# Kernel tuning notes

Measured on AMD Instinct MI355X. Metric: run time of the kernel, lower is better.

The kernel has to match this reference:

```python
import jax, jax.numpy as jnp
import numpy as np

B, T = 32, 64
DETER, HID, STOCH, CLASSES = 2048, 1024, 32, 32
ACT, EMB, BLOCKS = 16, 1024, 8
FLAT = STOCH * CLASSES
DPB = DETER // BLOCKS
DYN_IN_PB = DPB + 3 * HID
EPS = 1e-6
UNIMIX = 0.01


def _rms(x, g):
    return x * jax.lax.rsqrt(jnp.mean(x * x, axis=-1, keepdims=True) + EPS) * g


def _block_linear(x, W, b):
    # x: [N, BLOCKS*in_pb], W: [BLOCKS, in_pb, out_pb] -> [N, BLOCKS*out_pb]
    xg = x.reshape(x.shape[0], BLOCKS, -1)
    y = jnp.einsum('nbi,bio->nbo', xg, W)
    return y.reshape(x.shape[0], -1) + b


def setup_inputs() -> dict:
    key = jax.random.key(0)
    ks = iter(jax.random.split(key, 64))
    def lin(i, o):
        return jax.random.normal(next(ks), (i, o), jnp.float32) / np.float32(np.sqrt(i))
    inp = {}
    inp['embed'] = jax.random.normal(next(ks), (B, T, EMB), jnp.float32)
    inp['action'] = jax.random.normal(next(ks), (B, T, ACT), jnp.float32)
    inp['is_first'] = jax.random.randint(next(ks), (B, T), 0, 2).astype(jnp.int32)
    inp['W_in_deter'] = lin(DETER, HID); inp['b_in_deter'] = jnp.zeros((HID,), jnp.float32); inp['g_in_deter'] = jnp.ones((HID,), jnp.float32)
    inp['W_in_stoch'] = lin(FLAT, HID); inp['b_in_stoch'] = jnp.zeros((HID,), jnp.float32); inp['g_in_stoch'] = jnp.ones((HID,), jnp.float32)
    inp['W_in_act'] = lin(ACT, HID); inp['b_in_act'] = jnp.zeros((HID,), jnp.float32); inp['g_in_act'] = jnp.ones((HID,), jnp.float32)
    inp['W_dyn'] = jax.random.normal(next(ks), (BLOCKS, DYN_IN_PB, DPB), jnp.float32) / np.float32(np.sqrt(DYN_IN_PB))
    inp['b_dyn'] = jnp.zeros((DETER,), jnp.float32); inp['g_dyn'] = jnp.ones((DETER,), jnp.float32)
    inp['W_gru'] = jax.random.normal(next(ks), (BLOCKS, DPB, 3 * DPB), jnp.float32) / np.float32(np.sqrt(DPB))
    inp['b_gru'] = jnp.zeros((3 * DETER,), jnp.float32)
    inp['W_p0'] = lin(DETER, HID); inp['b_p0'] = jnp.zeros((HID,), jnp.float32); inp['g_p0'] = jnp.ones((HID,), jnp.float32)
    inp['W_p1'] = lin(HID, HID); inp['b_p1'] = jnp.zeros((HID,), jnp.float32); inp['g_p1'] = jnp.ones((HID,), jnp.float32)
    inp['W_po'] = jax.random.uniform(next(ks), (HID, FLAT), jnp.float32, -1.0, 1.0) / np.float32(np.sqrt(HID))
    inp['b_po'] = jnp.zeros((FLAT,), jnp.float32)
    inp['W_q0'] = lin(DETER + EMB, HID); inp['b_q0'] = jnp.zeros((HID,), jnp.float32); inp['g_q0'] = jnp.ones((HID,), jnp.float32)
    inp['W_qo'] = jax.random.uniform(next(ks), (HID, FLAT), jnp.float32, -1.0, 1.0) / np.float32(np.sqrt(HID))
    inp['b_qo'] = jnp.zeros((FLAT,), jnp.float32)
    return inp


def reference(embed, action, is_first,
              W_in_deter, b_in_deter, g_in_deter,
              W_in_stoch, b_in_stoch, g_in_stoch,
              W_in_act, b_in_act, g_in_act,
              W_dyn, b_dyn, g_dyn, W_gru, b_gru,
              W_p0, b_p0, g_p0, W_p1, b_p1, g_p1, W_po, b_po,
              W_q0, b_q0, g_q0, W_qo, b_qo):

    def core(deter, stoch_flat, act):
        denom = jax.lax.stop_gradient(jnp.maximum(jnp.abs(act), 1.0))
        a = act / denom
        x0 = jax.nn.silu(_rms(deter @ W_in_deter + b_in_deter, g_in_deter))
        x1 = jax.nn.silu(_rms(stoch_flat @ W_in_stoch + b_in_stoch, g_in_stoch))
        x2 = jax.nn.silu(_rms(a @ W_in_act + b_in_act, g_in_act))
        x = jnp.concatenate([x0, x1, x2], axis=-1)  # [B, 3H]
        xb = jnp.broadcast_to(x[:, None, :], (x.shape[0], BLOCKS, 3 * HID))
        dg = deter.reshape(-1, BLOCKS, DPB)
        h = jnp.concatenate([dg, xb], axis=-1).reshape(x.shape[0], -1)
        h = jax.nn.silu(_rms(_block_linear(h, W_dyn, b_dyn), g_dyn))
        gates = _block_linear(h, W_gru, b_gru).reshape(-1, BLOCKS, 3 * DPB)
        r = jax.nn.sigmoid(gates[..., :DPB])
        c = jnp.tanh(r * gates[..., DPB:2 * DPB])
        u = jax.nn.sigmoid(gates[..., 2 * DPB:] - 1.0)
        return (u * c + (1.0 - u) * dg).reshape(-1, DETER)

    def prior(deter):
        x = jax.nn.silu(_rms(deter @ W_p0 + b_p0, g_p0))
        x = jax.nn.silu(_rms(x @ W_p1 + b_p1, g_p1))
        return (x @ W_po + b_po).reshape(-1, STOCH, CLASSES)

    def post(deter, emb):
        x = jnp.concatenate([deter, emb], axis=-1)
        x = jax.nn.silu(_rms(x @ W_q0 + b_q0, g_q0))
        return (x @ W_qo + b_qo).reshape(-1, STOCH, CLASSES)

    def mode_st(logits):
        # unimix categorical, deterministic mode with straight-through gradients
        probs = (1.0 - UNIMIX) * jax.nn.softmax(logits, axis=-1) + UNIMIX / CLASSES
        onehot = jax.nn.one_hot(jnp.argmax(probs, axis=-1), CLASSES, dtype=probs.dtype)
        return onehot + probs - jax.lax.stop_gradient(probs)

    def step(carry, xs):
        deter, stoch = carry
        emb_t, act_t, first_t = xs
        m = (1.0 - first_t.astype(jnp.float32))[:, None]
        deter = deter * m
        stoch = stoch * m
        act_t = act_t * m
        deter = core(deter, stoch, act_t)
        prior_logits = prior(deter)
        post_logits = post(deter, emb_t)
        stoch = mode_st(post_logits).reshape(-1, FLAT)
        return (deter, stoch), (post_logits, prior_logits, deter)

    carry0 = (jnp.zeros((B, DETER), embed.dtype), jnp.zeros((B, FLAT), embed.dtype))
    xs = (embed.transpose(1, 0, 2), action.transpose(1, 0, 2), is_first.T)
    _, (post_l, prior_l, deters) = jax.lax.scan(step, carry0, xs)
    return (post_l.transpose(1, 0, 2, 3), prior_l.transpose(1, 0, 2, 3), deters.transpose(1, 0, 2))
```

## Files before the change

kernel.cpp:

```cpp
#include <hip/hip_runtime.h>
#include <math.h>

#define DEVINL __device__ __forceinline__
typedef float f32x4 __attribute__((ext_vector_type(4)));


struct RPtrs {
  const float *embed, *action; const int *is_first;
  const float *W_in_deter, *b_in_deter, *g_in_deter;
  const float *W_in_stoch, *b_in_stoch, *g_in_stoch;
  const float *W_in_act,   *b_in_act,   *g_in_act;
  const float *W_dyn, *b_dyn, *g_dyn;
  const float *W_gru, *b_gru;
  const float *W_p0, *b_p0, *g_p0;
  const float *W_p1, *b_p1, *g_p1;
  const float *W_po, *b_po;
  const float *W_q0, *b_q0, *g_q0;
  const float *W_qo, *b_qo;
  float *out_post, *out_prior, *out_deters;
  float *deter, *determ, *xact, *hact;
  float *SDyn, *SQ0, *SX0, *Abuf0, *Abuf1;
  int *sidxg;
};

struct LdPlain {
  const float* A; int lda;
  DEVINL const float* addr(int r, int k) const { return A + (size_t)r * lda + k; }
};
struct LdDyn {
  const float* dm; const float* x; int blk;
  DEVINL const float* addr(int r, int k) const {
    return (k < 256) ? dm + (size_t)r * 2048 + blk * 256 + k
                     : x + (size_t)r * 3072 + (k - 256);
  }
};
struct LdQ0 {
  const float* det; const float* emb; int t;
  DEVINL const float* addr(int r, int k) const {
    return (k < 2048) ? det + (size_t)r * 2048 + k
                      : emb + ((size_t)r * 64 + t) * 1024 + (k - 2048);
  }
};

#define FMA4(A, S, W) { (A)[0]=fmaf((S),(W)[0],(A)[0]); (A)[1]=fmaf((S),(W)[1],(A)[1]); \
                        (A)[2]=fmaf((S),(W)[2],(A)[2]); (A)[3]=fmaf((S),(W)[3],(A)[3]); }

template <int NBLK, typename LA>
DEVINL void gemm_tile(LA la, const float* __restrict__ W, int ldw, int wcb,
                      int k0, float* __restrict__ slab, int sst, int scb,
                      const float* __restrict__ bias, float* As) {
  const int tid = threadIdx.x;
  const int c4 = (tid & 63) * 4;
  const int rg = (tid >> 6) * 8;
  const int srr = tid & 31;
  const int skk = (tid >> 5) * 8;
  f32x4 acc[8];
#pragma unroll
  for (int i = 0; i < 8; ++i) acc[i] = (f32x4){0.f, 0.f, 0.f, 0.f};
  const float* ap = la.addr(srr, k0 + skk);
  f32x4 cur0 = *(const f32x4*)ap;
  f32x4 cur1 = *(const f32x4*)(ap + 4);
#pragma unroll
  for (int b = 0; b < NBLK; ++b) {
    __syncthreads();
#pragma unroll
    for (int e = 0; e < 4; ++e) {
      As[(skk + e) * 36 + srr]     = cur0[e];
      As[(skk + 4 + e) * 36 + srr] = cur1[e];
    }
    f32x4 nxt0, nxt1;
    if (b + 1 < NBLK) {
      const float* np = la.addr(srr, k0 + (b + 1) * 64 + skk);
      nxt0 = *(const f32x4*)np;
      nxt1 = *(const f32x4*)(np + 4);
    }
    __syncthreads();
    const float* Wp = W + (size_t)(k0 + b * 64) * ldw + wcb + c4;
#pragma unroll 8
    for (int kk = 0; kk < 64; ++kk) {
      f32x4 w = *(const f32x4*)(Wp + (size_t)kk * ldw);
      const float* Ab = As + kk * 36 + rg;
      f32x4 alo = *(const f32x4*)(Ab);
      f32x4 ahi = *(const f32x4*)(Ab + 4);
      FMA4(acc[0], alo[0], w); FMA4(acc[1], alo[1], w);
      FMA4(acc[2], alo[2], w); FMA4(acc[3], alo[3], w);
      FMA4(acc[4], ahi[0], w); FMA4(acc[5], ahi[1], w);
      FMA4(acc[6], ahi[2], w); FMA4(acc[7], ahi[3], w);
    }
    if (b + 1 < NBLK) { cur0 = nxt0; cur1 = nxt1; }
  }
  f32x4 bv = (f32x4){0.f, 0.f, 0.f, 0.f};
  if (bias) bv = *(const f32x4*)(bias + wcb + c4);
#pragma unroll
  for (int i = 0; i < 8; ++i) {
    f32x4 o = acc[i] + bv;
    *(f32x4*)(slab + (size_t)(rg + i) * sst + scb + c4) = o;
  }
}

template <typename LA>
DEVINL void gemm_big(LA la, const float* __restrict__ W, int ldw, int wcb,
                     int nblk, float* __restrict__ outp, int ost,
                     const float* __restrict__ bias, float* As) {
  const int tid = threadIdx.x;
  const int c4 = (tid & 63) * 4;
  const int rg = (tid >> 6) * 8;
  const int srr = tid & 31;
  const int skk = (tid >> 5) * 8;
  f32x4 acc[8];
#pragma unroll
  for (int i = 0; i < 8; ++i) acc[i] = (f32x4){0.f, 0.f, 0.f, 0.f};
  const float* ap = la.addr(srr, skk);
  f32x4 cur0 = *(const f32x4*)ap;
  f32x4 cur1 = *(const f32x4*)(ap + 4);
  f32x4 nxt0, nxt1;
  for (int b = 0; b < nblk; ++b) {
    __syncthreads();
#pragma unroll
    for (int e = 0; e < 4; ++e) {
      As[(skk + e) * 36 + srr]     = cur0[e];
      As[(skk + 4 + e) * 36 + srr] = cur1[e];
    }
    if (b + 1 < nblk) {
      const float* np = la.addr(srr, (b + 1) * 64 + skk);
      nxt0 = *(const f32x4*)np;
      nxt1 = *(const f32x4*)(np + 4);
    }
    __syncthreads();
    const float* Wp = W + (size_t)(b * 64) * ldw + wcb + c4;
#pragma unroll 8
    for (int kk = 0; kk < 64; ++kk) {
      f32x4 w = *(const f32x4*)(Wp + (size_t)kk * ldw);
      const float* Ab = As + kk * 36 + rg;
      f32x4 alo = *(const f32x4*)(Ab);
      f32x4 ahi = *(const f32x4*)(Ab + 4);
      FMA4(acc[0], alo[0], w); FMA4(acc[1], alo[1], w);
      FMA4(acc[2], alo[2], w); FMA4(acc[3], alo[3], w);
      FMA4(acc[4], ahi[0], w); FMA4(acc[5], ahi[1], w);
      FMA4(acc[6], ahi[2], w); FMA4(acc[7], ahi[3], w);
    }
    if (b + 1 < nblk) { cur0 = nxt0; cur1 = nxt1; }
  }
  f32x4 bv = *(const f32x4*)(bias + wcb + c4);
#pragma unroll
  for (int i = 0; i < 8; ++i) {
    f32x4 o = acc[i] + bv;
    *(f32x4*)(outp + (size_t)(rg + i) * ost + wcb + c4) = o;
  }
}

DEVINL void act_fin(const float* __restrict__ slab, int N, int nch, int r,
                    const float* __restrict__ g, float* __restrict__ out,
                    float invN, float* red) {
  const int tid = threadIdx.x;
  const size_t cstr = (size_t)32 * N;
  const float* base = slab + (size_t)r * N + tid * 4;
  f32x4 y0 = (f32x4){0.f, 0.f, 0.f, 0.f}, y1 = y0;
  for (int ch = 0; ch < nch; ++ch)
    y0 += *(const f32x4*)(base + (size_t)ch * cstr);
  float ss = y0[0]*y0[0] + y0[1]*y0[1] + y0[2]*y0[2] + y0[3]*y0[3];
  if (N == 2048) {
    for (int ch = 0; ch < nch; ++ch)
      y1 += *(const f32x4*)(base + 1024 + (size_t)ch * cstr);
    ss += y1[0]*y1[0] + y1[1]*y1[1] + y1[2]*y1[2] + y1[3]*y1[3];
  }
#pragma unroll
  for (int o = 32; o > 0; o >>= 1) ss += __shfl_down(ss, o, 64);
  if ((tid & 63) == 0) red[tid >> 6] = ss;
  __syncthreads();
  if (tid == 0)
    red[4] = 1.f / sqrtf((red[0] + red[1] + red[2] + red[3]) * invN + 1e-6f);
  __syncthreads();
  const float sc = red[4];
  {
    f32x4 gg = *(const f32x4*)(g + tid * 4);
    f32x4 v = y0 * sc * gg;
#pragma unroll
    for (int k = 0; k < 4; ++k) v[k] = v[k] / (1.f + expf(-v[k]));
    *(f32x4*)(out + tid * 4) = v;
  }
  if (N == 2048) {
    f32x4 gg = *(const f32x4*)(g + 1024 + tid * 4);
    f32x4 v = y1 * sc * gg;
#pragma unroll
    for (int k = 0; k < 4; ++k) v[k] = v[k] / (1.f + expf(-v[k]));
    *(f32x4*)(out + 1024 + tid * 4) = v;
  }
}

DEVINL float sigm(float x) { return 1.f / (1.f + expf(-x)); }

DEVINL void x2_row(const RPtrs& p, int tt, int r, float m, float* red) {
  const int tid = threadIdx.x;
  const int c0 = tid * 4;
  const float* arow = p.action + ((size_t)r * 64 + tt) * 16;
  f32x4 s2 = *(const f32x4*)(p.b_in_act + c0);
#pragma unroll
  for (int ii = 0; ii < 16; ++ii) {
    float av = arow[ii] * m;
    av = av / fmaxf(fabsf(av), 1.f);
    f32x4 wv = *(const f32x4*)(p.W_in_act + ii * 1024 + c0);
    FMA4(s2, av, wv);
  }
  float ss = s2[0]*s2[0] + s2[1]*s2[1] + s2[2]*s2[2] + s2[3]*s2[3];
#pragma unroll
  for (int o = 32; o > 0; o >>= 1) ss += __shfl_down(ss, o, 64);
  if ((tid & 63) == 0) red[tid >> 6] = ss;
  __syncthreads();
  if (tid == 0)
    red[4] = 1.f / sqrtf((red[0] + red[1] + red[2] + red[3]) * (1.f / 1024.f) + 1e-6f);
  __syncthreads();
  float sc = red[4];
  f32x4 gg = *(const f32x4*)(p.g_in_act + c0);
  f32x4 v = s2 * sc * gg;
#pragma unroll
  for (int k = 0; k < 4; ++k) v[k] = v[k] / (1.f + expf(-v[k]));
  *(f32x4*)(p.xact + (size_t)r * 3072 + 2048 + c0) = v;
}

DEVINL void bias_row(const float* __restrict__ b, const float* __restrict__ g,
                     float* __restrict__ out, float* red) {
  const int tid = threadIdx.x;
  const int c0 = tid * 4;
  f32x4 pre = *(const f32x4*)(b + c0);
  float ss = pre[0]*pre[0] + pre[1]*pre[1] + pre[2]*pre[2] + pre[3]*pre[3];
#pragma unroll
  for (int o = 32; o > 0; o >>= 1) ss += __shfl_down(ss, o, 64);
  if ((tid & 63) == 0) red[tid >> 6] = ss;
  __syncthreads();
  if (tid == 0)
    red[4] = 1.f / sqrtf((red[0] + red[1] + red[2] + red[3]) * (1.f / 1024.f) + 1e-6f);
  __syncthreads();
  float sc = red[4];
  f32x4 gg = *(const f32x4*)(g + c0);
  f32x4 v = pre * sc * gg;
#pragma unroll
  for (int k = 0; k < 4; ++k) v[k] = v[k] / (1.f + expf(-v[k]));
  *(f32x4*)(out + c0) = v;
}

__global__ __launch_bounds__(256) void k_init(RPtrs p) {
  __shared__ float red[8];
  const int wg = blockIdx.x;
  size_t i = (size_t)wg * 256 + threadIdx.x;
  if (i < 65536) { p.deter[i] = 0.f; p.determ[i] = 0.f; }
  if (wg >= 480) {
    const int r = wg - 480;
    bias_row(p.b_in_deter, p.g_in_deter, p.xact + (size_t)r * 3072, red);
    __syncthreads();
    bias_row(p.b_in_stoch, p.g_in_stoch, p.xact + (size_t)r * 3072 + 1024, red);
    __syncthreads();
    float m = p.is_first[r * 64] ? 0.f : 1.f;
    x2_row(p, 0, r, m, red);
  }
}

__global__ __launch_bounds__(256, 2) void k_dyn(RPtrs p, int t) {
  __shared__ __align__(16) float As[2304];
  const int wg = blockIdx.x;
  int blk = wg / 26, kc = wg % 26;
  LdDyn la{p.determ, p.xact, blk};
  gemm_tile<2>(la, p.W_dyn + (size_t)blk * 851968, 256, 0, kc * 128,
               p.SDyn + (size_t)kc * 65536, 2048, blk * 256,
               kc == 0 ? p.b_dyn + blk * 256 : nullptr, As);
}

__global__ __launch_bounds__(256, 2) void k_dynfin(RPtrs p) {
  __shared__ float red[8];
  act_fin(p.SDyn, 2048, 26, blockIdx.x, p.g_dyn,
          p.hact + (size_t)blockIdx.x * 2048, 1.f / 2048.f, red);
}

__global__ __launch_bounds__(256, 2) void k_gru(RPtrs p, int t) {
  __shared__ float Al[8704];
  const int wg = blockIdx.x;
  const int blk = wg >> 4, jch = wg & 15;
  const int tid = threadIdx.x;
  {
    const float* hp = p.hact + blk * 256 + tid;
#pragma unroll
    for (int jb = 0; jb < 32; ++jb)
      Al[tid * 34 + jb] = hp[(size_t)jb * 2048];
  }
  __syncthreads();
  const int j = tid & 15, rg = tid >> 4;
  const int r0 = rg * 2;
  const int jcol = jch * 16 + j;
  const float* Wg = p.W_gru + (size_t)blk * 196608 + jcol;
  float r0a = 0, r1a = 0, c0a = 0, c1a = 0, u0a = 0, u1a = 0;
#pragma unroll 4
  for (int kk = 0; kk < 256; ++kk) {
    float wr = Wg[(size_t)kk * 768];
    float wc = Wg[(size_t)kk * 768 + 256];
    float wu = Wg[(size_t)kk * 768 + 512];
    float ax = Al[kk * 34 + r0], ay = Al[kk * 34 + r0 + 1];
    r0a = fmaf(ax, wr, r0a); r1a = fmaf(ay, wr, r1a);
    c0a = fmaf(ax, wc, c0a); c1a = fmaf(ay, wc, c1a);
    u0a = fmaf(ax, wu, u0a); u1a = fmaf(ay, wu, u1a);
  }
  const int col = blk * 256 + jcol;
  const float br = p.b_gru[blk * 768 + jcol];
  const float bc = p.b_gru[blk * 768 + 256 + jcol];
  const float bu = p.b_gru[blk * 768 + 512 + jcol];
#pragma unroll
  for (int rr = 0; rr < 2; ++rr) {
    int r = r0 + rr;
    float gr = (rr ? r1a : r0a) + br;
    float gc = (rr ? c1a : c0a) + bc;
    float gu = (rr ? u1a : u0a) + bu;
    float rs = sigm(gr);
    float cc = tanhf(rs * gc);
    float uu = sigm(gu - 1.f);
    float dg = p.determ[(size_t)r * 2048 + col];
    float nd = uu * cc + (1.f - uu) * dg;
    p.deter[(size_t)r * 2048 + col] = nd;
    p.out_deters[((size_t)r * 64 + t) * 2048 + col] = nd;
    float mn = 0.f;
    if (t + 1 < 64) mn = p.is_first[r * 64 + (t + 1)] ? 0.f : 1.f;
    p.determ[(size_t)r * 2048 + col] = nd * mn;
  }
}

__global__ __launch_bounds__(256, 2) void k_q0x0(RPtrs p, int t) {
  __shared__ __align__(16) float As[2304];
  const int wg = blockIdx.x;
  if (wg < 96) {
    int ct = wg & 3, kc = wg >> 2;
    LdQ0 la{p.deter, p.embed, t};
    gemm_tile<2>(la, p.W_q0, 1024, ct * 256, kc * 128,
                 p.SQ0 + (size_t)kc * 32768, 1024, ct * 256,
                 kc == 0 ? p.b_q0 : nullptr, As);
  } else {
    if (t >= 63) return;
    int i = wg - 96, ct = i & 3, kc = i >> 2;
    LdPlain la{p.determ, 2048};
    gemm_tile<2>(la, p.W_in_deter, 1024, ct * 256, kc * 128,
                 p.SX0 + (size_t)kc * 32768, 1024, ct * 256,
                 kc == 0 ? p.b_in_deter : nullptr, As);
  }
}

__global__ __launch_bounds__(256, 2) void k_qo256(RPtrs p, int t) {
  __shared__ __align__(16) float smem[2184];
  float* qrow = smem;
  float* pbuf = smem + 1024;
  float* ybuf = smem + 2048;
  float* red  = smem + 2176;
  const int wg = blockIdx.x;
  const int r = wg >> 3, ch = wg & 7;
  const int tid = threadIdx.x;
  const int c0 = tid * 4;
  {
    const float* base = p.SQ0 + (size_t)r * 1024 + c0;
    f32x4 y = (f32x4){0.f, 0.f, 0.f, 0.f};
#pragma unroll
    for (int cc = 0; cc < 24; ++cc) y += *(const f32x4*)(base + (size_t)cc * 32768);
    float ss = y[0]*y[0] + y[1]*y[1] + y[2]*y[2] + y[3]*y[3];
#pragma unroll
    for (int o = 32; o > 0; o >>= 1) ss += __shfl_down(ss, o, 64);
    if ((tid & 63) == 0) red[tid >> 6] = ss;
    __syncthreads();
    if (tid == 0)
      red[4] = 1.f / sqrtf((red[0] + red[1] + red[2] + red[3]) * (1.f / 1024.f) + 1e-6f);
    __syncthreads();
    float sc = red[4];
    f32x4 gg = *(const f32x4*)(p.g_q0 + c0);
    f32x4 v = y * sc * gg;
#pragma unroll
    for (int k = 0; k < 4; ++k) v[k] = v[k] / (1.f + expf(-v[k]));
    *(f32x4*)(qrow + c0) = v;
  }
  __syncthreads();
  const int cg = tid & 31, ks = tid >> 5;
  {
    f32x4 acc = (f32x4){0.f, 0.f, 0.f, 0.f};
    const float* Wq = p.W_qo + ch * 128 + cg * 4;
    const float* qr = qrow + ks * 128;
#pragma unroll 8
    for (int k = 0; k < 128; ++k) {
      f32x4 wv = *(const f32x4*)(Wq + (size_t)(ks * 128 + k) * 1024);
      FMA4(acc, qr[k], wv);
    }
    *(f32x4*)(pbuf + (ks * 32 + cg) * 4) = acc;
  }
  __syncthreads();
  if (tid < 32) {
    f32x4 s = *(const f32x4*)(p.b_qo + ch * 128 + tid * 4);
#pragma unroll
    for (int k2 = 0; k2 < 8; ++k2) s += *(const f32x4*)(pbuf + (k2 * 32 + tid) * 4);
    *(f32x4*)(p.out_post + ((size_t)r * 64 + t) * 1024 + ch * 128 + tid * 4) = s;
    *(f32x4*)(ybuf + tid * 4) = s;
  }
  __syncthreads();
  if (t < 63 && tid < 4) {
    const float* rb = ybuf + tid * 32;
    float best = rb[0]; int bi = 0;
#pragma unroll
    for (int c = 1; c < 32; ++c) {
      float v = rb[c];
      if (v > best) { best = v; bi = c; }
    }
    p.sidxg[r * 32 + ch * 4 + tid] = bi;
  }
}

__global__ __launch_bounds__(256, 2) void k_finx12(RPtrs p, int t) {
  __shared__ float red[8];
  __shared__ int sidx[32];
  const int wg = blockIdx.x;
  const int tid = threadIdx.x;
  if (wg >= 32) {
    act_fin(p.SX0, 1024, 16, wg - 32, p.g_in_deter,
            p.xact + (size_t)(wg - 32) * 3072, 1.f / 1024.f, red);
    return;
  }
  const int r = wg;
  if (tid < 32) sidx[tid] = p.sidxg[r * 32 + tid] & 31;
  __syncthreads();
  const float m = p.is_first[r * 64 + t + 1] ? 0.f : 1.f;
  const int c0 = tid * 4;
  f32x4 s1 = (f32x4){0.f, 0.f, 0.f, 0.f};
  if (m != 0.f) {
    for (int g = 0; g < 32; ++g)
      s1 += *(const f32x4*)(p.W_in_stoch + (size_t)(g * 32 + sidx[g]) * 1024 + c0);
  }
  f32x4 pre = *(const f32x4*)(p.b_in_stoch + c0) + s1 * m;
  float ss = pre[0]*pre[0] + pre[1]*pre[1] + pre[2]*pre[2] + pre[3]*pre[3];
#pragma unroll
  for (int o = 32; o > 0; o >>= 1) ss += __shfl_down(ss, o, 64);
  if ((tid & 63) == 0) red[tid >> 6] = ss;
  __syncthreads();
  if (tid == 0)
    red[4] = 1.f / sqrtf((red[0] + red[1] + red[2] + red[3]) * (1.f / 1024.f) + 1e-6f);
  __syncthreads();
  {
    float sc = red[4];
    f32x4 gg = *(const f32x4*)(p.g_in_stoch + c0);
    f32x4 v = pre * sc * gg;
#pragma unroll
    for (int k = 0; k < 4; ++k) v[k] = v[k] / (1.f + expf(-v[k]));
    *(f32x4*)(p.xact + (size_t)r * 3072 + 1024 + c0) = v;
  }
  __syncthreads();
  x2_row(p, t + 1, r, m, red);
}

__global__ __launch_bounds__(256, 2) void kb_p0(RPtrs p) {
  __shared__ __align__(16) float As[2304];
  int rb = blockIdx.x >> 2, ct = blockIdx.x & 3;
  LdPlain la{p.out_deters + (size_t)rb * 32 * 2048, 2048};
  gemm_big(la, p.W_p0, 1024, ct * 256, 32,
           p.Abuf0 + (size_t)rb * 32 * 1024, 1024, p.b_p0, As);
}
__global__ __launch_bounds__(256, 2) void kb_fin0(RPtrs p) {
  __shared__ float red[8];
  int r = blockIdx.x;
  act_fin(p.Abuf0, 1024, 1, r, p.g_p0, p.Abuf1 + (size_t)r * 1024,
          1.f / 1024.f, red);
}
__global__ __launch_bounds__(256, 2) void kb_p1(RPtrs p) {
  __shared__ __align__(16) float As[2304];
  int rb = blockIdx.x >> 2, ct = blockIdx.x & 3;
  LdPlain la{p.Abuf1 + (size_t)rb * 32 * 1024, 1024};
  gemm_big(la, p.W_p1, 1024, ct * 256, 16,
           p.Abuf0 + (size_t)rb * 32 * 1024, 1024, p.b_p1, As);
}
__global__ __launch_bounds__(256, 2) void kb_fin1(RPtrs p) {
  __shared__ float red[8];
  int r = blockIdx.x;
  act_fin(p.Abuf0, 1024, 1, r, p.g_p1, p.Abuf1 + (size_t)r * 1024,
          1.f / 1024.f, red);
}
__global__ __launch_bounds__(256, 2) void kb_po(RPtrs p) {
  __shared__ __align__(16) float As[2304];
  int rb = blockIdx.x >> 2, ct = blockIdx.x & 3;
  LdPlain la{p.Abuf1 + (size_t)rb * 32 * 1024, 1024};
  gemm_big(la, p.W_po, 1024, ct * 256, 16,
           p.out_prior + (size_t)rb * 32 * 1024, 1024, p.b_po, As);
}

extern "C" void kernel_launch(void* const* d_in, const int* in_sizes, int n_in,
                              void* d_out, int out_size, void* d_ws,
                              size_t ws_size, hipStream_t stream) {
  RPtrs p;
  p.embed      = (const float*)d_in[0];
  p.action     = (const float*)d_in[1];
  p.is_first   = (const int*)d_in[2];
  p.W_in_deter = (const float*)d_in[3];  p.b_in_deter = (const float*)d_in[4];  p.g_in_deter = (const float*)d_in[5];
  p.W_in_stoch = (const float*)d_in[6];  p.b_in_stoch = (const float*)d_in[7];  p.g_in_stoch = (const float*)d_in[8];
  p.W_in_act   = (const float*)d_in[9];  p.b_in_act   = (const float*)d_in[10]; p.g_in_act   = (const float*)d_in[11];
  p.W_dyn      = (const float*)d_in[12]; p.b_dyn      = (const float*)d_in[13]; p.g_dyn      = (const float*)d_in[14];
  p.W_gru      = (const float*)d_in[15]; p.b_gru      = (const float*)d_in[16];
  p.W_p0       = (const float*)d_in[17]; p.b_p0       = (const float*)d_in[18]; p.g_p0       = (const float*)d_in[19];
  p.W_p1       = (const float*)d_in[20]; p.b_p1       = (const float*)d_in[21]; p.g_p1       = (const float*)d_in[22];
  p.W_po       = (const float*)d_in[23]; p.b_po       = (const float*)d_in[24];
  p.W_q0       = (const float*)d_in[25]; p.b_q0       = (const float*)d_in[26]; p.g_q0       = (const float*)d_in[27];
  p.W_qo       = (const float*)d_in[28]; p.b_qo       = (const float*)d_in[29];

  float* o = (float*)d_out;
  p.out_post   = o;
  p.out_prior  = o + 2097152;
  p.out_deters = o + 4194304;

  float* w = (float*)d_ws;
  p.deter  = w;
  p.determ = w + 65536;
  p.xact   = w + 131072;
  p.hact   = w + 229376;
  p.SDyn   = w + 393216;
  p.SQ0    = w + 2097152;
  p.SX0    = w + 2883584;
  p.Abuf0  = w;
  p.Abuf1  = w + 2097152;
  p.sidxg  = (int*)(w + 4194304);

  k_init<<<512, 256, 0, stream>>>(p);
  for (int t = 0; t < 64; ++t) {
    k_dyn<<<208, 256, 0, stream>>>(p, t);
    k_dynfin<<<32, 256, 0, stream>>>(p);
    k_gru<<<128, 256, 0, stream>>>(p, t);
    k_q0x0<<<160, 256, 0, stream>>>(p, t);
    k_qo256<<<256, 256, 0, stream>>>(p, t);
    if (t < 63) k_finx12<<<64, 256, 0, stream>>>(p, t);
  }
  kb_p0<<<256, 256, 0, stream>>>(p);
  kb_fin0<<<2048, 256, 0, stream>>>(p);
  kb_p1<<<256, 256, 0, stream>>>(p);
  kb_fin1<<<2048, 256, 0, stream>>>(p);
  kb_po<<<256, 256, 0, stream>>>(p);
}
```

Before: 6.935 ms.

## Enlarge post-scan GEMM row tile to 64 and move x0 finalize into qo kernel

The post-scan prior MLP GEMMs now compute 64 rows per block with 16 accumulators per thread instead of 32 rows, halving block count and doubling reuse of each weight load. The fin kernels each process 8 rows per block to cut block count. The in_deter act_fin work moves from k_finx12 into extra blocks of k_qo256, so it overlaps with the qo work and k_finx12 runs fewer blocks. The larger tile raises register pressure and lowers parallelism (128 blocks on a large GPU).

After: 7.397 ms. +6.7%, slower.

```diff
diff --git a/kernel.cpp b/kernel.cpp
--- a/kernel.cpp
+++ b/kernel.cpp
@@ -99,51 +99,63 @@
 }
 
 template <typename LA>
-DEVINL void gemm_big(LA la, const float* __restrict__ W, int ldw, int wcb,
-                     int nblk, float* __restrict__ outp, int ost,
-                     const float* __restrict__ bias, float* As) {
+DEVINL void gemm_big64(LA la, const float* __restrict__ W, int ldw, int wcb,
+                       int nblk, float* __restrict__ outp, int ost,
+                       const float* __restrict__ bias, float* As) {
   const int tid = threadIdx.x;
   const int c4 = (tid & 63) * 4;
-  const int rg = (tid >> 6) * 8;
-  const int srr = tid & 31;
-  const int skk = (tid >> 5) * 8;
-  f32x4 acc[8];
-#pragma unroll
-  for (int i = 0; i < 8; ++i) acc[i] = (f32x4){0.f, 0.f, 0.f, 0.f};
+  const int rg = (tid >> 6) * 16;
+  const int srr = tid & 63;
+  const int skk = (tid >> 6) * 16;
+  f32x4 acc[16];
+#pragma unroll
+  for (int i = 0; i < 16; ++i) acc[i] = (f32x4){0.f, 0.f, 0.f, 0.f};
   const float* ap = la.addr(srr, skk);
   f32x4 cur0 = *(const f32x4*)ap;
   f32x4 cur1 = *(const f32x4*)(ap + 4);
-  f32x4 nxt0, nxt1;
+  f32x4 cur2 = *(const f32x4*)(ap + 8);
+  f32x4 cur3 = *(const f32x4*)(ap + 12);
   for (int b = 0; b < nblk; ++b) {
     __syncthreads();
 #pragma unroll
     for (int e = 0; e < 4; ++e) {
-      As[(skk + e) * 36 + srr]     = cur0[e];
-      As[(skk + 4 + e) * 36 + srr] = cur1[e];
-    }
+      As[(skk + e) * 68 + srr]      = cur0[e];
+      As[(skk + 4 + e) * 68 + srr]  = cur1[e];
+      As[(skk + 8 + e) * 68 + srr]  = cur2[e];
+      As[(skk + 12 + e) * 68 + srr] = cur3[e];
+    }
+    f32x4 nxt0, nxt1, nxt2, nxt3;
     if (b + 1 < nblk) {
       const float* np = la.addr(srr, (b + 1) * 64 + skk);
       nxt0 = *(const f32x4*)np;
       nxt1 = *(const f32x4*)(np + 4);
+      nxt2 = *(const f32x4*)(np + 8);
+      nxt3 = *(const f32x4*)(np + 12);
     }
     __syncthreads();
     const float* Wp = W + (size_t)(b * 64) * ldw + wcb + c4;
-#pragma unroll 8
+#pragma unroll 4
     for (int kk = 0; kk < 64; ++kk) {
       f32x4 w = *(const f32x4*)(Wp + (size_t)kk * ldw);
-      const float* Ab = As + kk * 36 + rg;
-      f32x4 alo = *(const f32x4*)(Ab);
-      f32x4 ahi = *(const f32x4*)(Ab + 4);
-      FMA4(acc[0], alo[0], w); FMA4(acc[1], alo[1], w);
-      FMA4(acc[2], alo[2], w); FMA4(acc[3], alo[3], w);
-      FMA4(acc[4], ahi[0], w); FMA4(acc[5], ahi[1], w);
-      FMA4(acc[6], ahi[2], w); FMA4(acc[7], ahi[3], w);
-    }
-    if (b + 1 < nblk) { cur0 = nxt0; cur1 = nxt1; }
+      const float* Ab = As + kk * 68 + rg;
+      f32x4 a0 = *(const f32x4*)(Ab);
+      f32x4 a1 = *(const f32x4*)(Ab + 4);
+      f32x4 a2 = *(const f32x4*)(Ab + 8);
+      f32x4 a3 = *(const f32x4*)(Ab + 12);
+      FMA4(acc[0],  a0[0], w); FMA4(acc[1],  a0[1], w);
+      FMA4(acc[2],  a0[2], w); FMA4(acc[3],  a0[3], w);
+      FMA4(acc[4],  a1[0], w); FMA4(acc[5],  a1[1], w);
+      FMA4(acc[6],  a1[2], w); FMA4(acc[7],  a1[3], w);
+      FMA4(acc[8],  a2[0], w); FMA4(acc[9],  a2[1], w);
+      FMA4(acc[10], a2[2], w); FMA4(acc[11], a2[3], w);
+      FMA4(acc[12], a3[0], w); FMA4(acc[13], a3[1], w);
+      FMA4(acc[14], a3[2], w); FMA4(acc[15], a3[3], w);
+    }
+    if (b + 1 < nblk) { cur0 = nxt0; cur1 = nxt1; cur2 = nxt2; cur3 = nxt3; }
   }
   f32x4 bv = *(const f32x4*)(bias + wcb + c4);
 #pragma unroll
-  for (int i = 0; i < 8; ++i) {
+  for (int i = 0; i < 16; ++i) {
     f32x4 o = acc[i] + bv;
     *(f32x4*)(outp + (size_t)(rg + i) * ost + wcb + c4) = o;
   }
@@ -186,6 +198,7 @@
     for (int k = 0; k < 4; ++k) v[k] = v[k] / (1.f + expf(-v[k]));
     *(f32x4*)(out + 1024 + tid * 4) = v;
   }
+  __syncthreads();
 }
 
 DEVINL float sigm(float x) { return 1.f / (1.f + expf(-x)); }
@@ -342,13 +355,19 @@
 
 __global__ __launch_bounds__(256, 2) void k_qo256(RPtrs p, int t) {
   __shared__ __align__(16) float smem[2184];
+  const int wg = blockIdx.x;
+  const int tid = threadIdx.x;
+  if (wg >= 256) {
+    if (t >= 63) return;
+    act_fin(p.SX0, 1024, 16, wg - 256, p.g_in_deter,
+            p.xact + (size_t)(wg - 256) * 3072, 1.f / 1024.f, smem);
+    return;
+  }
   float* qrow = smem;
   float* pbuf = smem + 1024;
   float* ybuf = smem + 2048;
   float* red  = smem + 2176;
-  const int wg = blockIdx.x;
   const int r = wg >> 3, ch = wg & 7;
-  const int tid = threadIdx.x;
   const int c0 = tid * 4;
   {
     const float* base = p.SQ0 + (size_t)r * 1024 + c0;
@@ -407,14 +426,8 @@
 __global__ __launch_bounds__(256, 2) void k_finx12(RPtrs p, int t) {
   __shared__ float red[8];
   __shared__ int sidx[32];
-  const int wg = blockIdx.x;
-  const int tid = threadIdx.x;
-  if (wg >= 32) {
-    act_fin(p.SX0, 1024, 16, wg - 32, p.g_in_deter,
-            p.xact + (size_t)(wg - 32) * 3072, 1.f / 1024.f, red);
-    return;
-  }
-  const int r = wg;
+  const int r = blockIdx.x;
+  const int tid = threadIdx.x;
   if (tid < 32) sidx[tid] = p.sidxg[r * 32 + tid] & 31;
   __syncthreads();
   const float m = p.is_first[r * 64 + t + 1] ? 0.f : 1.f;
@@ -446,37 +459,41 @@
 }
 
 __global__ __launch_bounds__(256, 2) void kb_p0(RPtrs p) {
-  __shared__ __align__(16) float As[2304];
+  __shared__ __align__(16) float As[4352];
   int rb = blockIdx.x >> 2, ct = blockIdx.x & 3;
-  LdPlain la{p.out_deters + (size_t)rb * 32 * 2048, 2048};
-  gemm_big(la, p.W_p0, 1024, ct * 256, 32,
-           p.Abuf0 + (size_t)rb * 32 * 1024, 1024, p.b_p0, As);
+  LdPlain la{p.out_deters + (size_t)rb * 64 * 2048, 2048};
+  gemm_big64(la, p.W_p0, 1024, ct * 256, 32,
+             p.Abuf0 + (size_t)rb * 64 * 1024, 1024, p.b_p0, As);
 }
 __global__ __launch_bounds__(256, 2) void kb_fin0(RPtrs p) {
   __shared__ float red[8];
-  int r = blockIdx.x;
-  act_fin(p.Abuf0, 1024, 1, r, p.g_p0, p.Abuf1 + (size_t)r * 1024,
-          1.f / 1024.f, red);
+  for (int i = 0; i < 8; ++i) {
+    int r = blockIdx.x * 8 + i;
+    act_fin(p.Abuf0, 1024, 1, r, p.g_p0, p.Abuf1 + (size_t)r * 1024,
+            1.f / 1024.f, red);
+  }
 }
 __global__ __launch_bounds__(256, 2) void kb_p1(RPtrs p) {
-  __shared__ __align__(16) float As[2304];
+  __shared__ __align__(16) float As[4352];
   int rb = blockIdx.x >> 2, ct = blockIdx.x & 3;
-  LdPlain la{p.Abuf1 + (size_t)rb * 32 * 1024, 1024};
-  gemm_big(la, p.W_p1, 1024, ct * 256, 16,
-           p.Abuf0 + (size_t)rb * 32 * 1024, 1024, p.b_p1, As);
+  LdPlain la{p.Abuf1 + (size_t)rb * 64 * 1024, 1024};
+  gemm_big64(la, p.W_p1, 1024, ct * 256, 16,
+             p.Abuf0 + (size_t)rb * 64 * 1024, 1024, p.b_p1, As);
 }
 __global__ __launch_bounds__(256, 2) void kb_fin1(RPtrs p) {
   __shared__ float red[8];
-  int r = blockIdx.x;
-  act_fin(p.Abuf0, 1024, 1, r, p.g_p1, p.Abuf1 + (size_t)r * 1024,
-          1.f / 1024.f, red);
+  for (int i = 0; i < 8; ++i) {
+    int r = blockIdx.x * 8 + i;
+    act_fin(p.Abuf0, 1024, 1, r, p.g_p1, p.Abuf1 + (size_t)r * 1024,
+            1.f / 1024.f, red);
+  }
 }
 __global__ __launch_bounds__(256, 2) void kb_po(RPtrs p) {
-  __shared__ __align__(16) float As[2304];
+  __shared__ __align__(16) float As[4352];
   int rb = blockIdx.x >> 2, ct = blockIdx.x & 3;
-  LdPlain la{p.Abuf1 + (size_t)rb * 32 * 1024, 1024};
-  gemm_big(la, p.W_po, 1024, ct * 256, 16,
-           p.out_prior + (size_t)rb * 32 * 1024, 1024, p.b_po, As);
+  LdPlain la{p.Abuf1 + (size_t)rb * 64 * 1024, 1024};
+  gemm_big64(la, p.W_po, 1024, ct * 256, 16,
+             p.out_prior + (size_t)rb * 64 * 1024, 1024, p.b_po, As);
 }
 
 extern "C" void kernel_launch(void* const* d_in, const int* in_sizes, int n_in,
@@ -520,12 +537,12 @@
     k_dynfin<<<32, 256, 0, stream>>>(p);
     k_gru<<<128, 256, 0, stream>>>(p, t);
     k_q0x0<<<160, 256, 0, stream>>>(p, t);
-    k_qo256<<<256, 256, 0, stream>>>(p, t);
-    if (t < 63) k_finx12<<<64, 256, 0, stream>>>(p, t);
-  }
-  kb_p0<<<256, 256, 0, stream>>>(p);
-  kb_fin0<<<2048, 256, 0, stream>>>(p);
-  kb_p1<<<256, 256, 0, stream>>>(p);
-  kb_fin1<<<2048, 256, 0, stream>>>(p);
-  kb_po<<<256, 256, 0, stream>>>(p);
-}
+    k_qo256<<<288, 256, 0, stream>>>(p, t);
+    if (t < 63) k_finx12<<<32, 256, 0, stream>>>(p, t);
+  }
+  kb_p0<<<128, 256, 0, stream>>>(p);
+  kb_fin0<<<256, 256, 0, stream>>>(p);
+  kb_p1<<<128, 256, 0, stream>>>(p);
+  kb_fin1<<<256, 256, 0, stream>>>(p);
+  kb_po<<<128, 256, 0, stream>>>(p);
+}
```
